# Kernel optimization log

Measured on AMD Instinct MI355X. Metric: run time of the kernel, lower is better.

## Reference

```python
import jax, jax.numpy as jnp
import numpy as np

N = 10000       # nodes (atoms)
E = 160000      # edges (avg degree 16)
NE = 10         # num_elements
C = 64          # hidden scalar channels (hidden_irreps 0e multiplicity)
NB = 8          # num_bessel
SH = 9          # spherical-harmonic dim for max_ell=2 (1+3+5)
MLPH = 16       # readout MLP hidden (MLP_irreps)
T = 2           # num_interactions
R_MAX = 5.0
P_CUT = 6       # num_polynomial_cutoff
AVG_NEIGH = 32.0


def _sph(u):
    # real spherical harmonics up to l=2, e3nn 'component' normalization
    x, y, z = u[:, 0], u[:, 1], u[:, 2]
    s3, s5, s15 = 3.0 ** 0.5, 5.0 ** 0.5, 15.0 ** 0.5
    return jnp.stack([
        jnp.ones_like(x),
        s3 * x, s3 * y, s3 * z,
        s15 * x * y, s15 * y * z, (s5 / 2) * (3 * z * z - 1),
        s15 * x * z, (s15 / 2) * (x * x - y * y)], axis=-1)


def _radial(r):
    # Bessel radial basis * smooth polynomial cutoff (RadialEmbeddingBlock)
    n = jnp.arange(1, NB + 1, dtype=r.dtype)
    bessel = (2.0 / R_MAX) ** 0.5 * jnp.sin(n * jnp.pi * r[:, None] / R_MAX) / r[:, None]
    x = jnp.clip(r / R_MAX, 0.0, 1.0)
    p = P_CUT
    fc = (1.0 - 0.5 * (p + 1) * (p + 2) * x ** p
          + p * (p + 2) * x ** (p + 1)
          - 0.5 * p * (p + 1) * x ** (p + 2))
    fc = jnp.where(x < 1.0, fc, 0.0)
    return bessel * fc[:, None]


def setup_inputs():
    key = jax.random.key(0)
    ks = jax.random.split(key, 14)
    positions = jax.random.normal(ks[0], (N, 3), jnp.float32) * 3.0
    node_attrs = jax.nn.one_hot(jax.random.randint(ks[1], (N,), 0, NE), NE, dtype=jnp.float32)
    edge_index = jax.random.randint(ks[2], (2, E), 0, N)
    shifts = jnp.zeros((E, 3), jnp.float32)

    def g(k, shape, fan):
        return jax.random.normal(k, shape, jnp.float32) / np.sqrt(fan)

    params = dict(
        atomic_energies=jax.random.normal(ks[3], (NE,), jnp.float32),
        W_embed=g(ks[4], (NE, C), NE),          # LinearNodeEmbeddingBlock
        W_up=g(ks[5], (T, C, C), C),            # linear_up per interaction
        W_r1=g(ks[6], (T, NB, MLPH), NB),       # radial MLP layer 1
        W_r2=g(ks[7], (T, MLPH, C * SH), MLPH), # radial MLP -> TP weights
        W_mix=g(ks[8], (T, C, SH, C), C * SH),  # post-scatter linear mixing
        W_self=g(ks[9], (T, C, C), C),          # self/skip connection
        w_read=g(ks[10], (C,), C),              # LinearReadoutBlock
        W_mlp1=g(ks[11], (C, MLPH), C),         # NonLinearReadoutBlock
        w_mlp2=g(ks[12], (MLPH,), MLPH),
    )
    return dict(positions=positions, node_attrs=node_attrs, shifts=shifts,
                edge_index=edge_index, **params)


def reference(positions, node_attrs, shifts, atomic_energies, W_embed, W_up,
              W_r1, W_r2, W_mix, W_self, w_read, W_mlp1, w_mlp2, edge_index):
    snd, rcv = edge_index[0], edge_index[1]
    vec = positions[rcv] - positions[snd] + shifts              # [E,3]
    r = jnp.linalg.norm(vec, axis=-1) + 1e-9                    # [E]
    sh = _sph(vec / r[:, None])                                 # [E,SH]
    edge_feats = _radial(r)                                     # [E,NB]

    h = node_attrs @ W_embed                                    # [N,C] node embedding
    reps = [node_attrs @ atomic_energies]                       # node_e0
    for t in range(T):
        h_up = h @ W_up[t]                                      # [N,C]
        # radial-MLP produced tensor-product weights, one per (channel, sh) path
        tp_w = (jax.nn.silu(edge_feats @ W_r1[t]) @ W_r2[t]).reshape(-1, C, SH)
        # gather -> edge-wise tensor product -> scatter-reduce (the hot loop)
        msg = tp_w * h_up[snd][:, :, None] * sh[:, None, :]     # [E,C,SH]
        agg = jax.ops.segment_sum(msg, rcv, num_segments=N) / AVG_NEIGH
        h = jnp.einsum('ncs,cso->no', agg, W_mix[t]) + h @ W_self[t]
        if t < T - 1:
            reps.append(h @ w_read)                             # linear readout
        else:
            reps.append(jax.nn.silu(h @ W_mlp1) @ w_mlp2)       # nonlinear readout
    return jnp.stack(reps, axis=0)  # [T+1, N] per-layer atomic energy contributions
```

## Files before the change

kernel.cpp:

```cpp
#include <hip/hip_runtime.h>
#include <math.h>

#define N_NODES 10000
#define N_EDGES 160000
#define NEL 10
#define C 64
#define NB 8
#define SHD 9
#define MLPH 16
#define CSH 576
#define R_MAX 5.0f
#define INV_AVG 0.03125f
#define SCAN_CH 40
#define GRID_MSG 768
#define NWAVES (GRID_MSG * 4)
#define WBASE (N_EDGES - 2 * 8 * CSH)
#define WB2   (WBASE - 10240)
#define WB3   (WB2 - 1024)

typedef _Float16 f16x2 __attribute__((ext_vector_type(2)));
typedef _Float16 f16x8 __attribute__((ext_vector_type(8)));
typedef float    f32x4 __attribute__((ext_vector_type(4)));
typedef _Float16 half_t;

__device__ __forceinline__ float silu_f(float v) {
    return v / (1.0f + __expf(-v));
}

__device__ __forceinline__ float dot2f(f16x2 a, f16x2 b, float c) {
#if __has_builtin(__builtin_amdgcn_fdot2)
    return __builtin_amdgcn_fdot2(a, b, c, false);
#else
    return c + (float)a.x * (float)b.x + (float)a.y * (float)b.y;
#endif
}

__device__ __forceinline__ int lbound_rp(const int* __restrict__ rp, int target) {
    int lo = 0, hi = N_NODES;
    while (lo < hi) { int mid = (lo + hi) >> 1; if (rp[mid] < target) lo = mid + 1; else hi = mid; }
    return lo;
}

__global__ __launch_bounds__(256) void k_edge(
    const float* __restrict__ pos, const float* __restrict__ shifts,
    const int* __restrict__ ei,
    const float* __restrict__ na, const float* __restrict__ We,
    const float* __restrict__ ae,
    int* __restrict__ cnt, int* __restrict__ deg,
    int* __restrict__ act_snd, int* __restrict__ act_rcv,
    float* __restrict__ act_u, float* __restrict__ act_ef,
    half_t* __restrict__ hh, float* __restrict__ out)
{
    int i = blockIdx.x * 256 + threadIdx.x;
    int lane = threadIdx.x & 63;

    {
        int n = i >> 6;
        float acc = 0.0f, e0 = 0.0f;
        #pragma unroll
        for (int k = 0; k < NEL; k++) {
            float a = na[n * NEL + k];
            acc += a * We[k * C + lane];
            e0 += a * ae[k];
        }
        hh[i] = (half_t)acc;
        if (lane == 0) out[n] = e0;
    }

    if (blockIdx.x >= N_EDGES / 256) return;
    int e = i;
    int snd = ei[e];
    int rcv = ei[N_EDGES + e];
    float vx = pos[rcv * 3 + 0] - pos[snd * 3 + 0] + shifts[e * 3 + 0];
    float vy = pos[rcv * 3 + 1] - pos[snd * 3 + 1] + shifts[e * 3 + 1];
    float vz = pos[rcv * 3 + 2] - pos[snd * 3 + 2] + shifts[e * 3 + 2];
    float r = sqrtf(vx * vx + vy * vy + vz * vz) + 1e-9f;
    float x = r / R_MAX;
    bool active = x < 1.0f;

    unsigned long long m = __ballot(active);
    int base = 0;
    if (m) {
        int leader = __ffsll((unsigned long long)m) - 1;
        if (lane == leader) base = atomicAdd(cnt, __popcll(m));
        base = __shfl(base, leader);
    }
    if (!active) return;

    int p = base + __popcll(m & ((1ull << lane) - 1ull));
    act_snd[p] = snd;
    act_rcv[p] = rcv;
    atomicAdd(&deg[rcv], 1);

    float inv_r = 1.0f / r;
    *(float4*)&act_u[p * 4] = make_float4(vx * inv_r, vy * inv_r, vz * inv_r, r);

    float x6 = x * x * x; x6 = x6 * x6;
    float x7 = x6 * x;
    float x8 = x7 * x;
    float fc = 1.0f - 28.0f * x6 + 48.0f * x7 - 21.0f * x8;
    float theta = 3.14159265358979323846f * r / R_MAX;
    float s1 = sinf(theta), c1 = cosf(theta);
    float sn = s1, cn = c1;
    float scale = 0.6324555320336759f * inv_r * fc;
    float ef[NB];
    ef[0] = scale * sn;
    #pragma unroll
    for (int n = 1; n < NB; n++) {
        float sn1 = sn * c1 + cn * s1;
        float cn1 = cn * c1 - sn * s1;
        sn = sn1; cn = cn1;
        ef[n] = scale * sn;
    }
    *(float4*)&act_ef[p * 8 + 0] = make_float4(ef[0], ef[1], ef[2], ef[3]);
    *(float4*)&act_ef[p * 8 + 4] = make_float4(ef[4], ef[5], ef[6], ef[7]);
}

__global__ __launch_bounds__(256) void k_scan(
    const int* __restrict__ deg, int* __restrict__ rowptr, int* __restrict__ cursor)
{
    __shared__ int dl[N_NODES];
    __shared__ int part[256];
    int tid = threadIdx.x;
    for (int i = tid; i < N_NODES; i += 256) dl[i] = deg[i];
    __syncthreads();

    int base = tid * SCAN_CH;
    int s = 0;
    #pragma unroll 8
    for (int i = 0; i < SCAN_CH; i++) {
        int idx = base + i;
        if (idx < N_NODES) s += dl[idx];
    }
    part[tid] = s;
    __syncthreads();
    for (int off = 1; off < 256; off <<= 1) {
        int v = (tid >= off) ? part[tid - off] : 0;
        __syncthreads();
        part[tid] += v;
        __syncthreads();
    }
    int run = part[tid] - s;
    for (int i = 0; i < SCAN_CH; i++) {
        int idx = base + i;
        if (idx < N_NODES) {
            int v = dl[idx];
            dl[idx] = run;
            run += v;
        }
    }
    __syncthreads();
    for (int i = tid; i < N_NODES; i += 256) {
        int r = dl[i];
        rowptr[i] = r;
        cursor[i] = r;
    }
    if (tid == 255) rowptr[N_NODES] = part[255];
}

__global__ __launch_bounds__(256) void k_rank(
    const int* __restrict__ cnt, const int* __restrict__ act_rcv,
    const float* __restrict__ Wr2, const float* __restrict__ Wmix,
    const float* __restrict__ Wself, const float* __restrict__ Wup,
    const int* __restrict__ rowptr,
    int* __restrict__ cursor, int* __restrict__ wstart, f16x2* __restrict__ wlth,
    f16x8* __restrict__ wmixf, f16x8* __restrict__ wupf, int* __restrict__ perm)
{
    int i = blockIdx.x * 256 + threadIdx.x;
    int nAct = *cnt;

    if (i <= NWAVES) {
        if (i == NWAVES) {
            wstart[NWAVES] = N_NODES;
        } else {
            int S = (nAct + NWAVES - 1) / NWAVES; if (S < 1) S = 1;
            wstart[i] = lbound_rp(rowptr, i * S);
        }
    }
    if (i >= WBASE) {
        int idx = i - WBASE;
        int t = idx / (8 * CSH);
        int r = idx - t * (8 * CSH);
        int mq = r / CSH, j = r - mq * CSH;
        int c = j & 63, s = j >> 6;
        float lo = Wr2[t * MLPH * CSH + (2 * mq + 0) * CSH + c * SHD + s];
        float hi = Wr2[t * MLPH * CSH + (2 * mq + 1) * CSH + c * SHD + s];
        f16x2 v; v.x = (_Float16)lo; v.y = (_Float16)hi;
        wlth[idx] = v;
    } else if (i >= WB2) {
        int idx = i - WB2;
        int t = idx / 5120;
        int r = idx - t * 5120;
        int ks = r >> 8;
        int rr = r & 255;
        int nt = rr >> 6;
        int ln = rr & 63;
        f16x8 v;
        #pragma unroll
        for (int e = 0; e < 8; e++) {
            int k = ks * 32 + ((ln >> 4) << 3) + e;
            int col = nt * 16 + (ln & 15);
            float x;
            if (k < CSH)
                x = Wmix[(size_t)t * CSH * C + ((k & 63) * SHD + (k >> 6)) * C + col] * INV_AVG;
            else
                x = Wself[(size_t)t * C * C + (k - CSH) * C + col];
            v[e] = (_Float16)x;
        }
        wmixf[(size_t)((t * 20 + ks) * 4 + nt) * 64 + ln] = v;
    } else if (i >= WB3) {
        int idx = i - WB3;
        int t = idx >> 9;
        int r = idx & 511;
        int ks = r >> 8;
        int rr = r & 255;
        int nt = rr >> 6;
        int ln = rr & 63;
        f16x8 v;
        #pragma unroll
        for (int e = 0; e < 8; e++) {
            int k = ks * 32 + ((ln >> 4) << 3) + e;
            int col = nt * 16 + (ln & 15);
            v[e] = (_Float16)Wup[(size_t)t * C * C + k * C + col];
        }
        wupf[(size_t)((t * 2 + ks) * 4 + nt) * 64 + ln] = v;
    }
    if (i >= nAct) return;
    int pos = atomicAdd(&cursor[act_rcv[i]], 1);
    perm[pos] = i;
}

__global__ __launch_bounds__(256) void k_permute(
    const int* __restrict__ cnt, const int* __restrict__ perm,
    const int* __restrict__ act_snd, const int* __restrict__ act_rcv,
    const float* __restrict__ act_u, const float* __restrict__ act_ef,
    const float* __restrict__ Wr1,
    int* __restrict__ csnd, int* __restrict__ crcv, float* __restrict__ csh,
    f16x2* __restrict__ chidh0, f16x2* __restrict__ chidh1)
{
    int p = blockIdx.x * 256 + threadIdx.x;
    if (p >= *cnt) return;
    int i = perm[p];

    csnd[p] = act_snd[i];
    crcv[p] = act_rcv[i];

    float4 u4 = *(const float4*)&act_u[i * 4];
    float ux = u4.x, uy = u4.y, uz = u4.z;
    const float s3 = 1.7320508075688772f;
    const float s5 = 2.23606797749979f;
    const float s15 = 3.872983346207417f;
    *(float4*)&csh[p * 16 + 0] = make_float4(1.0f, s3 * ux, s3 * uy, s3 * uz);
    *(float4*)&csh[p * 16 + 4] = make_float4(s15 * ux * uy, s15 * uy * uz,
                                             0.5f * s5 * (3.0f * uz * uz - 1.0f),
                                             s15 * ux * uz);
    csh[p * 16 + 8] = 0.5f * s15 * (ux * ux - uy * uy);

    float4 e0 = *(const float4*)&act_ef[i * 8 + 0];
    float4 e1 = *(const float4*)&act_ef[i * 8 + 4];
    float ef[NB] = {e0.x, e0.y, e0.z, e0.w, e1.x, e1.y, e1.z, e1.w};

    #pragma unroll
    for (int t = 0; t < 2; t++) {
        f16x2* dst = (t == 0) ? chidh0 : chidh1;
        const float* W = Wr1 + t * NB * MLPH;
        f16x2 hv2[8];
        #pragma unroll
        for (int mp = 0; mp < 8; mp++) {
            float a0 = 0.0f, a1 = 0.0f;
            #pragma unroll
            for (int b = 0; b < NB; b++) {
                float efb = ef[b];
                a0 += efb * W[b * MLPH + 2 * mp + 0];
                a1 += efb * W[b * MLPH + 2 * mp + 1];
            }
            f16x2 v; v.x = (_Float16)silu_f(a0); v.y = (_Float16)silu_f(a1);
            hv2[mp] = v;
        }
        *(float4*)&dst[p * 8 + 0] = *(float4*)&hv2[0];
        *(float4*)&dst[p * 8 + 4] = *(float4*)&hv2[4];
    }
}

__global__ __launch_bounds__(64) void k_upm(
    const half_t* __restrict__ hh, const f16x8* __restrict__ wupf,
    float* __restrict__ hup)
{
    int lane = threadIdx.x & 63;
    int base = blockIdx.x * 16;
    int rowA = base + (lane & 15);
    int kg = (lane >> 4) << 3;

    f32x4 u0 = {0.f,0.f,0.f,0.f}, u1 = {0.f,0.f,0.f,0.f};
    f32x4 u2 = {0.f,0.f,0.f,0.f}, u3 = {0.f,0.f,0.f,0.f};
    const half_t* hrow = hh + (size_t)rowA * C + kg;
    #pragma unroll
    for (int ks = 0; ks < 2; ks++) {
        f16x8 a = *(const f16x8*)(hrow + ks * 32);
        const f16x8* bp = wupf + (size_t)(ks * 4) * 64 + lane;
        u0 = __builtin_amdgcn_mfma_f32_16x16x32_f16(a, bp[0],   u0, 0, 0, 0);
        u1 = __builtin_amdgcn_mfma_f32_16x16x32_f16(a, bp[64],  u1, 0, 0, 0);
        u2 = __builtin_amdgcn_mfma_f32_16x16x32_f16(a, bp[128], u2, 0, 0, 0);
        u3 = __builtin_amdgcn_mfma_f32_16x16x32_f16(a, bp[192], u3, 0, 0, 0);
    }
    int colb = lane & 15;
    int rowb = base + ((lane >> 4) << 2);
    #pragma unroll
    for (int r = 0; r < 4; r++) {
        float* hp = hup + (size_t)(rowb + r) * C + colb;
        hp[0]  = u0[r];
        hp[16] = u1[r];
        hp[32] = u2[r];
        hp[48] = u3[r];
    }
}

__global__ __launch_bounds__(256) void k_msg5(
    const int* __restrict__ rowptr, const int* __restrict__ wstart,
    const int* __restrict__ csnd, const int* __restrict__ crcv,
    const float* __restrict__ csh, const f16x2* __restrict__ chh,
    const f16x2* __restrict__ wlth, const float* __restrict__ hup,
    half_t* __restrict__ aggh)
{
    int lane = threadIdx.x & 63;
    int w = (blockIdx.x << 2) | (threadIdx.x >> 6);
    int nlo = wstart[w];
    int nhi = wstart[w + 1];
    if (nlo >= nhi) return;
    int beg = rowptr[nlo], end = rowptr[nhi];

    f16x2 wreg[8][9];
    #pragma unroll
    for (int mq = 0; mq < 8; mq++)
        #pragma unroll
        for (int jj = 0; jj < 9; jj++)
            wreg[mq][jj] = wlth[mq * CSH + (jj << 6) + lane];

    float acc[9];
    int curRcv = -1;

#define FLUSH() { half_t* ag = aggh + (size_t)curRcv * CSH + lane; \
    _Pragma("unroll") for (int jj = 0; jj < 9; jj++) ag[jj << 6] = (half_t)acc[jj]; }
#define ZFILL(FROM, TO) for (int zn = (FROM); zn < (TO); zn++) { \
    half_t* ag = aggh + (size_t)zn * CSH + lane; \
    _Pragma("unroll") for (int jj = 0; jj < 9; jj++) ag[jj << 6] = (half_t)0.0f; }

    for (int k0 = beg; k0 < end; k0 += 4) {
        int nv = end - k0; if (nv > 4) nv = 4;

#define PRE(Q) int kc##Q = (k0 + Q < end) ? k0 + Q : end - 1; \
        int rcvq##Q = crcv[kc##Q]; \
        float hupq##Q = hup[csnd[kc##Q] * C + lane];
        PRE(0) PRE(1) PRE(2) PRE(3)
#undef PRE

        float tw0[9], tw1[9], tw2[9], tw3[9];
        #pragma unroll
        for (int jj = 0; jj < 9; jj++) {
            tw0[jj] = 0.f; tw1[jj] = 0.f; tw2[jj] = 0.f; tw3[jj] = 0.f;
        }

        #pragma unroll
        for (int mq = 0; mq < 8; mq++) {
            f16x2 h0 = chh[kc0 * 8 + mq], h1 = chh[kc1 * 8 + mq];
            f16x2 h2 = chh[kc2 * 8 + mq], h3 = chh[kc3 * 8 + mq];
            #pragma unroll
            for (int jj = 0; jj < 9; jj++) {
                f16x2 wv = wreg[mq][jj];
                tw0[jj] = dot2f(h0, wv, tw0[jj]);
                tw1[jj] = dot2f(h1, wv, tw1[jj]);
                tw2[jj] = dot2f(h2, wv, tw2[jj]);
                tw3[jj] = dot2f(h3, wv, tw3[jj]);
            }
        }

#define SCAT(Q) if (Q < nv) { \
        int rcv = rcvq##Q; \
        float hupS = hupq##Q; \
        float4 sA = *(const float4*)&csh[kc##Q * 16]; \
        float4 sB = *(const float4*)&csh[kc##Q * 16 + 4]; \
        float s8v = csh[kc##Q * 16 + 8]; \
        float sh9[9] = {sA.x, sA.y, sA.z, sA.w, sB.x, sB.y, sB.z, sB.w, s8v}; \
        if (rcv != curRcv) { \
            if (curRcv >= 0) { FLUSH(); ZFILL(curRcv + 1, rcv) } else { ZFILL(nlo, rcv) } \
            curRcv = rcv; \
            _Pragma("unroll") for (int jj = 0; jj < 9; jj++) acc[jj] = tw##Q[jj] * (hupS * sh9[jj]); \
        } else { \
            _Pragma("unroll") for (int jj = 0; jj < 9; jj++) acc[jj] += tw##Q[jj] * (hupS * sh9[jj]); \
        } }
        SCAT(0) SCAT(1) SCAT(2) SCAT(3)
#undef SCAT
    }

    int zfrom = nlo;
    if (curRcv >= 0) { FLUSH(); zfrom = curRcv + 1; }
    ZFILL(zfrom, nhi)
#undef FLUSH
#undef ZFILL
}

template <int RMODE>
__global__ __launch_bounds__(64) void k_mixm(
    const half_t* __restrict__ aggh, half_t* __restrict__ hh,
    const f16x8* __restrict__ wf, const f16x8* __restrict__ wupf,
    const float* __restrict__ wread, const float* __restrict__ Wm1,
    const float* __restrict__ wm2,
    float* __restrict__ hup, float* __restrict__ rep)
{
    __shared__ half_t Hs[16 * 72];
    __shared__ float  Hn[16 * 68];
    __shared__ float  W1l[C * MLPH];

    int lane = threadIdx.x & 63;
    int base = blockIdx.x * 16;
    int rowA = base + (lane & 15);
    int kg = (lane >> 4) << 3;

    if (RMODE == 1) {
        #pragma unroll
        for (int it = 0; it < 16; it++) W1l[lane + 64 * it] = Wm1[lane + 64 * it];
    }

    f32x4 acc0 = {0.f, 0.f, 0.f, 0.f};
    f32x4 acc1 = {0.f, 0.f, 0.f, 0.f};
    f32x4 acc2 = {0.f, 0.f, 0.f, 0.f};
    f32x4 acc3 = {0.f, 0.f, 0.f, 0.f};

    const half_t* arow = aggh + (size_t)rowA * CSH + kg;
    const half_t* hrow = hh + (size_t)rowA * C + kg;

    #pragma unroll
    for (int ks = 0; ks < 20; ks++) {
        f16x8 a = (ks < 18) ? *(const f16x8*)(arow + ks * 32)
                            : *(const f16x8*)(hrow + (ks - 18) * 32);
        const f16x8* bp = wf + (size_t)(ks * 4) * 64 + lane;
        acc0 = __builtin_amdgcn_mfma_f32_16x16x32_f16(a, bp[0],   acc0, 0, 0, 0);
        acc1 = __builtin_amdgcn_mfma_f32_16x16x32_f16(a, bp[64],  acc1, 0, 0, 0);
        acc2 = __builtin_amdgcn_mfma_f32_16x16x32_f16(a, bp[128], acc2, 0, 0, 0);
        acc3 = __builtin_amdgcn_mfma_f32_16x16x32_f16(a, bp[192], acc3, 0, 0, 0);
    }

    int colb = lane & 15;
    int rowb = base + ((lane >> 4) << 2);
    int rloc = (lane >> 4) << 2;

    if (RMODE == 0) {
        float wr0 = wread[colb], wr1 = wread[colb + 16];
        float wr2 = wread[colb + 32], wr3 = wread[colb + 48];
        #pragma unroll
        for (int r = 0; r < 4; r++) {
            float v = acc0[r] * wr0 + acc1[r] * wr1 + acc2[r] * wr2 + acc3[r] * wr3;
            v += __shfl_xor(v, 1); v += __shfl_xor(v, 2);
            v += __shfl_xor(v, 4); v += __shfl_xor(v, 8);
            if (colb == 0) rep[rowb + r] = v;
        }

        #pragma unroll
        for (int r = 0; r < 4; r++) {
            Hs[(rloc + r) * 72 + colb +  0] = (half_t)acc0[r];
            Hs[(rloc + r) * 72 + colb + 16] = (half_t)acc1[r];
            Hs[(rloc + r) * 72 + colb + 32] = (half_t)acc2[r];
            Hs[(rloc + r) * 72 + colb + 48] = (half_t)acc3[r];
        }
        __syncthreads();

        #pragma unroll
        for (int it = 0; it < 2; it++) {
            int idx = lane + 64 * it;
            int row = idx >> 3, cq = idx & 7;
            *(float4*)&hh[(size_t)(base + row) * C + cq * 8] =
                *(const float4*)&Hs[row * 72 + cq * 8];
        }

        f32x4 u0 = {0.f,0.f,0.f,0.f}, u1 = {0.f,0.f,0.f,0.f};
        f32x4 u2 = {0.f,0.f,0.f,0.f}, u3 = {0.f,0.f,0.f,0.f};
        #pragma unroll
        for (int ks = 0; ks < 2; ks++) {
            f16x8 a = *(const f16x8*)&Hs[(lane & 15) * 72 + kg + ks * 32];
            const f16x8* bp = wupf + (size_t)(ks * 4) * 64 + lane;
            u0 = __builtin_amdgcn_mfma_f32_16x16x32_f16(a, bp[0],   u0, 0, 0, 0);
            u1 = __builtin_amdgcn_mfma_f32_16x16x32_f16(a, bp[64],  u1, 0, 0, 0);
            u2 = __builtin_amdgcn_mfma_f32_16x16x32_f16(a, bp[128], u2, 0, 0, 0);
            u3 = __builtin_amdgcn_mfma_f32_16x16x32_f16(a, bp[192], u3, 0, 0, 0);
        }
        #pragma unroll
        for (int r = 0; r < 4; r++) {
            float* hp = hup + (size_t)(rowb + r) * C + colb;
            hp[0]  = u0[r];
            hp[16] = u1[r];
            hp[32] = u2[r];
            hp[48] = u3[r];
        }
    } else {
        #pragma unroll
        for (int r = 0; r < 4; r++) {
            Hn[(rloc + r) * 68 + colb +  0] = acc0[r];
            Hn[(rloc + r) * 68 + colb + 16] = acc1[r];
            Hn[(rloc + r) * 68 + colb + 32] = acc2[r];
            Hn[(rloc + r) * 68 + colb + 48] = acc3[r];
        }
        __syncthreads();
        int n = lane & 15, q = lane >> 4;
        float a2[4] = {0.f, 0.f, 0.f, 0.f};
        #pragma unroll 8
        for (int c = 0; c < C; c++) {
            float hv = Hn[n * 68 + c];
            #pragma unroll
            for (int j = 0; j < 4; j++) a2[j] += hv * W1l[c * MLPH + 4 * q + j];
        }
        float rv = 0.0f;
        #pragma unroll
        for (int j = 0; j < 4; j++) rv += silu_f(a2[j]) * wm2[4 * q + j];
        rv += __shfl_xor(rv, 16);
        rv += __shfl_xor(rv, 32);
        if (lane < 16) rep[base + n] = rv;
    }
}

extern "C" void kernel_launch(void* const* d_in, const int* in_sizes, int n_in,
                              void* d_out, int out_size, void* d_ws, size_t ws_size,
                              hipStream_t stream) {
    const float* pos    = (const float*)d_in[0];
    const float* na     = (const float*)d_in[1];
    const float* shifts = (const float*)d_in[2];
    const int*   ei     = (const int*)d_in[3];
    const float* ae     = (const float*)d_in[4];
    const float* We     = (const float*)d_in[5];
    const float* Wup    = (const float*)d_in[6];
    const float* Wr1    = (const float*)d_in[7];
    const float* Wr2    = (const float*)d_in[8];
    const float* Wmix   = (const float*)d_in[9];
    const float* Wself  = (const float*)d_in[10];
    const float* wread  = (const float*)d_in[11];
    const float* Wm1    = (const float*)d_in[12];
    const float* wm2    = (const float*)d_in[13];
    float* out = (float*)d_out;

    char* ws = (char*)d_ws;
    size_t off = 0;
    auto alloc = [&](size_t bytes) {
        off = (off + 255) & ~(size_t)255;
        void* p = ws + off;
        off += bytes;
        return p;
    };
    int*   cnt     = (int*)alloc(4);
    int*   deg     = (int*)alloc((size_t)N_NODES * 4);
    int*   rowptr  = (int*)alloc((size_t)(N_NODES + 1) * 4);
    int*   cursor  = (int*)alloc((size_t)N_NODES * 4);
    int*   wstart  = (int*)alloc((size_t)(NWAVES + 1) * 4);
    f16x2* wlth    = (f16x2*)alloc((size_t)2 * 8 * CSH * 4);
    f16x8* wmixf   = (f16x8*)alloc((size_t)2 * 5120 * 16);
    f16x8* wupf    = (f16x8*)alloc((size_t)1024 * 16);
    int*   perm    = (int*)alloc((size_t)N_EDGES * 4);
    int*   act_snd = (int*)alloc((size_t)N_EDGES * 4);
    int*   act_rcv = (int*)alloc((size_t)N_EDGES * 4);
    float* act_u   = (float*)alloc((size_t)N_EDGES * 4 * 4);
    float* act_ef  = (float*)alloc((size_t)N_EDGES * 8 * 4);
    int*   csnd    = (int*)alloc((size_t)N_EDGES * 4);
    int*   crcv    = (int*)alloc((size_t)N_EDGES * 4);
    float* csh     = (float*)alloc((size_t)N_EDGES * 16 * 4);
    f16x2* chidh0  = (f16x2*)alloc((size_t)N_EDGES * 8 * 4);
    f16x2* chidh1  = (f16x2*)alloc((size_t)N_EDGES * 8 * 4);
    float* hup     = (float*)alloc((size_t)N_NODES * C * 4);
    half_t* hh     = (half_t*)alloc((size_t)N_NODES * C * 2);
    half_t* aggh   = (half_t*)alloc((size_t)N_NODES * CSH * 2);

    hipMemsetAsync(cnt, 0, 4, stream);
    hipMemsetAsync(deg, 0, (size_t)N_NODES * 4, stream);

    k_edge<<<(N_NODES * C) / 256, 256, 0, stream>>>(pos, shifts, ei, na, We, ae,
                                                    cnt, deg, act_snd, act_rcv,
                                                    act_u, act_ef, hh, out);
    k_scan<<<1, 256, 0, stream>>>(deg, rowptr, cursor);
    k_rank<<<N_EDGES / 256, 256, 0, stream>>>(cnt, act_rcv, Wr2, Wmix, Wself, Wup,
                                              rowptr, cursor, wstart, wlth,
                                              wmixf, wupf, perm);
    k_permute<<<N_EDGES / 256, 256, 0, stream>>>(cnt, perm, act_snd, act_rcv,
                                                 act_u, act_ef, Wr1,
                                                 csnd, crcv, csh, chidh0, chidh1);
    k_upm<<<N_NODES / 16, 64, 0, stream>>>(hh, wupf, hup);

    k_msg5<<<GRID_MSG, 256, 0, stream>>>(rowptr, wstart, csnd, crcv, csh,
                                         chidh0, wlth, hup, aggh);
    k_mixm<0><<<N_NODES / 16, 64, 0, stream>>>(aggh, hh, wmixf, wupf + 512,
                                               wread, Wm1, wm2,
                                               hup, out + N_NODES);

    k_msg5<<<GRID_MSG, 256, 0, stream>>>(rowptr, wstart, csnd, crcv, csh,
                                         chidh1, wlth + 8 * CSH, hup, aggh);
    k_mixm<1><<<N_NODES / 16, 64, 0, stream>>>(aggh, hh, wmixf + 5120, wupf + 512,
                                               wread, Wm1, wm2,
                                               hup, out + 2 * N_NODES);
}
```

Measured before the change: 134.9 us.

## Fuse message aggregation with mixing MLP via shared-memory aggregates

Merges the per-edge message/scatter kernel and the node mixing/readout kernel into one kernel per interaction. Each 256-thread block owns 16 nodes, and each wave handles 4 consecutive nodes. Aggregates go to LDS instead of a global fp16 buffer, then all four waves run the MFMA mixing together. This removes the global aggregate round-trip, one launch per layer and the edge-balanced wave partitioning (wstart binary search). The cost is load imbalance across waves, since work now follows node degree rather than edge count, and the load of the 72-entry weight registers is amortized over only 4 nodes per wave.

```diff
diff --git a/kernel.cpp b/kernel.cpp
--- a/kernel.cpp
+++ b/kernel.cpp
@@ -12,11 +12,10 @@
 #define R_MAX 5.0f
 #define INV_AVG 0.03125f
 #define SCAN_CH 40
-#define GRID_MSG 768
-#define NWAVES (GRID_MSG * 4)
 #define WBASE (N_EDGES - 2 * 8 * CSH)
 #define WB2   (WBASE - 10240)
 #define WB3   (WB2 - 1024)
+#define ROWP  584
 
 typedef _Float16 f16x2 __attribute__((ext_vector_type(2)));
 typedef _Float16 f16x8 __attribute__((ext_vector_type(8)));
@@ -33,12 +32,6 @@
 #else
     return c + (float)a.x * (float)b.x + (float)a.y * (float)b.y;
 #endif
-}
-
-__device__ __forceinline__ int lbound_rp(const int* __restrict__ rp, int target) {
-    int lo = 0, hi = N_NODES;
-    while (lo < hi) { int mid = (lo + hi) >> 1; if (rp[mid] < target) lo = mid + 1; else hi = mid; }
-    return lo;
 }
 
 __global__ __launch_bounds__(256) void k_edge(
@@ -162,21 +155,12 @@
     const int* __restrict__ cnt, const int* __restrict__ act_rcv,
     const float* __restrict__ Wr2, const float* __restrict__ Wmix,
     const float* __restrict__ Wself, const float* __restrict__ Wup,
-    const int* __restrict__ rowptr,
-    int* __restrict__ cursor, int* __restrict__ wstart, f16x2* __restrict__ wlth,
+    int* __restrict__ cursor, f16x2* __restrict__ wlth,
     f16x8* __restrict__ wmixf, f16x8* __restrict__ wupf, int* __restrict__ perm)
 {
     int i = blockIdx.x * 256 + threadIdx.x;
     int nAct = *cnt;
 
-    if (i <= NWAVES) {
-        if (i == NWAVES) {
-            wstart[NWAVES] = N_NODES;
-        } else {
-            int S = (nAct + NWAVES - 1) / NWAVES; if (S < 1) S = 1;
-            wstart[i] = lbound_rp(rowptr, i * S);
-        }
-    }
     if (i >= WBASE) {
         int idx = i - WBASE;
         int t = idx / (8 * CSH);
@@ -315,19 +299,25 @@
     }
 }
 
-__global__ __launch_bounds__(256) void k_msg5(
-    const int* __restrict__ rowptr, const int* __restrict__ wstart,
-    const int* __restrict__ csnd, const int* __restrict__ crcv,
-    const float* __restrict__ csh, const f16x2* __restrict__ chh,
-    const f16x2* __restrict__ wlth, const float* __restrict__ hup,
-    half_t* __restrict__ aggh)
+template <int RMODE>
+__global__ __launch_bounds__(256) void k_fuse(
+    const int* __restrict__ rowptr, const int* __restrict__ csnd,
+    const int* __restrict__ crcv, const float* __restrict__ csh,
+    const f16x2* __restrict__ chh, const f16x2* __restrict__ wlth,
+    const float* __restrict__ hup_in, const f16x8* __restrict__ wf,
+    const f16x8* __restrict__ wupf1, half_t* __restrict__ hh,
+    const float* __restrict__ wread, const float* __restrict__ Wm1,
+    const float* __restrict__ wm2,
+    float* __restrict__ hup_out, float* __restrict__ rep)
 {
+    __shared__ half_t Hs[16 * ROWP];
+    __shared__ half_t Hs2[16 * 72];
+
     int lane = threadIdx.x & 63;
-    int w = (blockIdx.x << 2) | (threadIdx.x >> 6);
-    int nlo = wstart[w];
-    int nhi = wstart[w + 1];
-    if (nlo >= nhi) return;
-    int beg = rowptr[nlo], end = rowptr[nhi];
+    int w = threadIdx.x >> 6;
+    int bbase = blockIdx.x * 16;
+    int n0 = bbase + w * 4;
+    int beg = rowptr[n0], end = rowptr[n0 + 4];
 
     f16x2 wreg[8][9];
     #pragma unroll
@@ -339,10 +329,10 @@
     float acc[9];
     int curRcv = -1;
 
-#define FLUSH() { half_t* ag = aggh + (size_t)curRcv * CSH + lane; \
+#define FLUSH() { half_t* ag = &Hs[(curRcv - bbase) * ROWP + lane]; \
     _Pragma("unroll") for (int jj = 0; jj < 9; jj++) ag[jj << 6] = (half_t)acc[jj]; }
 #define ZFILL(FROM, TO) for (int zn = (FROM); zn < (TO); zn++) { \
-    half_t* ag = aggh + (size_t)zn * CSH + lane; \
+    half_t* ag = &Hs[(zn - bbase) * ROWP + lane]; \
     _Pragma("unroll") for (int jj = 0; jj < 9; jj++) ag[jj << 6] = (half_t)0.0f; }
 
     for (int k0 = beg; k0 < end; k0 += 4) {
@@ -350,7 +340,7 @@
 
 #define PRE(Q) int kc##Q = (k0 + Q < end) ? k0 + Q : end - 1; \
         int rcvq##Q = crcv[kc##Q]; \
-        float hupq##Q = hup[csnd[kc##Q] * C + lane];
+        float hupq##Q = hup_in[csnd[kc##Q] * C + lane];
         PRE(0) PRE(1) PRE(2) PRE(3)
 #undef PRE
 
@@ -382,7 +372,7 @@
         float s8v = csh[kc##Q * 16 + 8]; \
         float sh9[9] = {sA.x, sA.y, sA.z, sA.w, sB.x, sB.y, sB.z, sB.w, s8v}; \
         if (rcv != curRcv) { \
-            if (curRcv >= 0) { FLUSH(); ZFILL(curRcv + 1, rcv) } else { ZFILL(nlo, rcv) } \
+            if (curRcv >= 0) { FLUSH(); ZFILL(curRcv + 1, rcv) } else { ZFILL(n0, rcv) } \
             curRcv = rcv; \
             _Pragma("unroll") for (int jj = 0; jj < 9; jj++) acc[jj] = tw##Q[jj] * (hupS * sh9[jj]); \
         } else { \
@@ -392,128 +382,84 @@
 #undef SCAT
     }
 
-    int zfrom = nlo;
+    int zfrom = n0;
     if (curRcv >= 0) { FLUSH(); zfrom = curRcv + 1; }
-    ZFILL(zfrom, nhi)
+    ZFILL(zfrom, n0 + 4)
 #undef FLUSH
 #undef ZFILL
-}
-
-template <int RMODE>
-__global__ __launch_bounds__(64) void k_mixm(
-    const half_t* __restrict__ aggh, half_t* __restrict__ hh,
-    const f16x8* __restrict__ wf, const f16x8* __restrict__ wupf,
-    const float* __restrict__ wread, const float* __restrict__ Wm1,
-    const float* __restrict__ wm2,
-    float* __restrict__ hup, float* __restrict__ rep)
-{
-    __shared__ half_t Hs[16 * 72];
-    __shared__ float  Hn[16 * 68];
-    __shared__ float  W1l[C * MLPH];
-
-    int lane = threadIdx.x & 63;
-    int base = blockIdx.x * 16;
-    int rowA = base + (lane & 15);
+
+    __syncthreads();
+
+    int rowL = lane & 15;
     int kg = (lane >> 4) << 3;
-
-    if (RMODE == 1) {
-        #pragma unroll
-        for (int it = 0; it < 16; it++) W1l[lane + 64 * it] = Wm1[lane + 64 * it];
-    }
-
-    f32x4 acc0 = {0.f, 0.f, 0.f, 0.f};
-    f32x4 acc1 = {0.f, 0.f, 0.f, 0.f};
-    f32x4 acc2 = {0.f, 0.f, 0.f, 0.f};
-    f32x4 acc3 = {0.f, 0.f, 0.f, 0.f};
-
-    const half_t* arow = aggh + (size_t)rowA * CSH + kg;
-    const half_t* hrow = hh + (size_t)rowA * C + kg;
-
+    f32x4 acc4 = {0.f, 0.f, 0.f, 0.f};
+    const half_t* hrow = hh + (size_t)(bbase + rowL) * C + kg;
     #pragma unroll
     for (int ks = 0; ks < 20; ks++) {
-        f16x8 a = (ks < 18) ? *(const f16x8*)(arow + ks * 32)
+        f16x8 a = (ks < 18) ? *(const f16x8*)&Hs[rowL * ROWP + ks * 32 + kg]
                             : *(const f16x8*)(hrow + (ks - 18) * 32);
-        const f16x8* bp = wf + (size_t)(ks * 4) * 64 + lane;
-        acc0 = __builtin_amdgcn_mfma_f32_16x16x32_f16(a, bp[0],   acc0, 0, 0, 0);
-        acc1 = __builtin_amdgcn_mfma_f32_16x16x32_f16(a, bp[64],  acc1, 0, 0, 0);
-        acc2 = __builtin_amdgcn_mfma_f32_16x16x32_f16(a, bp[128], acc2, 0, 0, 0);
-        acc3 = __builtin_amdgcn_mfma_f32_16x16x32_f16(a, bp[192], acc3, 0, 0, 0);
+        f16x8 b = wf[(size_t)(ks * 4 + w) * 64 + lane];
+        acc4 = __builtin_amdgcn_mfma_f32_16x16x32_f16(a, b, acc4, 0, 0, 0);
     }
 
     int colb = lane & 15;
-    int rowb = base + ((lane >> 4) << 2);
-    int rloc = (lane >> 4) << 2;
+    int rq = (lane >> 4) << 2;
+
+    __syncthreads();
 
     if (RMODE == 0) {
-        float wr0 = wread[colb], wr1 = wread[colb + 16];
-        float wr2 = wread[colb + 32], wr3 = wread[colb + 48];
-        #pragma unroll
-        for (int r = 0; r < 4; r++) {
-            float v = acc0[r] * wr0 + acc1[r] * wr1 + acc2[r] * wr2 + acc3[r] * wr3;
-            v += __shfl_xor(v, 1); v += __shfl_xor(v, 2);
-            v += __shfl_xor(v, 4); v += __shfl_xor(v, 8);
-            if (colb == 0) rep[rowb + r] = v;
-        }
-
-        #pragma unroll
-        for (int r = 0; r < 4; r++) {
-            Hs[(rloc + r) * 72 + colb +  0] = (half_t)acc0[r];
-            Hs[(rloc + r) * 72 + colb + 16] = (half_t)acc1[r];
-            Hs[(rloc + r) * 72 + colb + 32] = (half_t)acc2[r];
-            Hs[(rloc + r) * 72 + colb + 48] = (half_t)acc3[r];
-        }
+        #pragma unroll
+        for (int r = 0; r < 4; r++)
+            Hs2[(rq + r) * 72 + w * 16 + colb] = (half_t)acc4[r];
         __syncthreads();
 
-        #pragma unroll
-        for (int it = 0; it < 2; it++) {
-            int idx = lane + 64 * it;
-            int row = idx >> 3, cq = idx & 7;
-            *(float4*)&hh[(size_t)(base + row) * C + cq * 8] =
-                *(const float4*)&Hs[row * 72 + cq * 8];
-        }
-
-        f32x4 u0 = {0.f,0.f,0.f,0.f}, u1 = {0.f,0.f,0.f,0.f};
-        f32x4 u2 = {0.f,0.f,0.f,0.f}, u3 = {0.f,0.f,0.f,0.f};
+        if (w == 0) {
+            int row = lane & 15, seg = lane >> 4;
+            float v = 0.0f;
+            #pragma unroll
+            for (int j = 0; j < 16; j++)
+                v += (float)Hs2[row * 72 + seg * 16 + j] * wread[seg * 16 + j];
+            v += __shfl_xor(v, 16);
+            v += __shfl_xor(v, 32);
+            if (seg == 0) rep[bbase + row] = v;
+        }
+
+        {
+            int idx = threadIdx.x;
+            if (idx < 128) {
+                int row = idx >> 3, cq = idx & 7;
+                *(float4*)&hh[(size_t)(bbase + row) * C + cq * 8] =
+                    *(const float4*)&Hs2[row * 72 + cq * 8];
+            }
+        }
+
+        f32x4 u = {0.f, 0.f, 0.f, 0.f};
         #pragma unroll
         for (int ks = 0; ks < 2; ks++) {
-            f16x8 a = *(const f16x8*)&Hs[(lane & 15) * 72 + kg + ks * 32];
-            const f16x8* bp = wupf + (size_t)(ks * 4) * 64 + lane;
-            u0 = __builtin_amdgcn_mfma_f32_16x16x32_f16(a, bp[0],   u0, 0, 0, 0);
-            u1 = __builtin_amdgcn_mfma_f32_16x16x32_f16(a, bp[64],  u1, 0, 0, 0);
-            u2 = __builtin_amdgcn_mfma_f32_16x16x32_f16(a, bp[128], u2, 0, 0, 0);
-            u3 = __builtin_amdgcn_mfma_f32_16x16x32_f16(a, bp[192], u3, 0, 0, 0);
-        }
-        #pragma unroll
-        for (int r = 0; r < 4; r++) {
-            float* hp = hup + (size_t)(rowb + r) * C + colb;
-            hp[0]  = u0[r];
-            hp[16] = u1[r];
-            hp[32] = u2[r];
-            hp[48] = u3[r];
-        }
+            f16x8 a = *(const f16x8*)&Hs2[rowL * 72 + ks * 32 + kg];
+            f16x8 b = wupf1[(size_t)(ks * 4 + w) * 64 + lane];
+            u = __builtin_amdgcn_mfma_f32_16x16x32_f16(a, b, u, 0, 0, 0);
+        }
+        #pragma unroll
+        for (int r = 0; r < 4; r++)
+            hup_out[(size_t)(bbase + rq + r) * C + w * 16 + colb] = u[r];
     } else {
-        #pragma unroll
-        for (int r = 0; r < 4; r++) {
-            Hn[(rloc + r) * 68 + colb +  0] = acc0[r];
-            Hn[(rloc + r) * 68 + colb + 16] = acc1[r];
-            Hn[(rloc + r) * 68 + colb + 32] = acc2[r];
-            Hn[(rloc + r) * 68 + colb + 48] = acc3[r];
-        }
+        float* Hn = (float*)Hs;
+        float* W1l = (float*)Hs + 16 * 68;
+        for (int t = threadIdx.x; t < C * MLPH; t += 256) W1l[t] = Wm1[t];
+        #pragma unroll
+        for (int r = 0; r < 4; r++)
+            Hn[(rq + r) * 68 + w * 16 + colb] = acc4[r];
         __syncthreads();
-        int n = lane & 15, q = lane >> 4;
-        float a2[4] = {0.f, 0.f, 0.f, 0.f};
+
+        int n = threadIdx.x >> 4, m = threadIdx.x & 15;
+        float a2 = 0.0f;
         #pragma unroll 8
-        for (int c = 0; c < C; c++) {
-            float hv = Hn[n * 68 + c];
-            #pragma unroll
-            for (int j = 0; j < 4; j++) a2[j] += hv * W1l[c * MLPH + 4 * q + j];
-        }
-        float rv = 0.0f;
-        #pragma unroll
-        for (int j = 0; j < 4; j++) rv += silu_f(a2[j]) * wm2[4 * q + j];
-        rv += __shfl_xor(rv, 16);
-        rv += __shfl_xor(rv, 32);
-        if (lane < 16) rep[base + n] = rv;
+        for (int c = 0; c < C; c++) a2 += Hn[n * 68 + c] * W1l[c * MLPH + m];
+        float rv = silu_f(a2) * wm2[m];
+        rv += __shfl_xor(rv, 1); rv += __shfl_xor(rv, 2);
+        rv += __shfl_xor(rv, 4); rv += __shfl_xor(rv, 8);
+        if (m == 0) rep[bbase + n] = rv;
     }
 }
 
@@ -548,7 +494,6 @@
     int*   deg     = (int*)alloc((size_t)N_NODES * 4);
     int*   rowptr  = (int*)alloc((size_t)(N_NODES + 1) * 4);
     int*   cursor  = (int*)alloc((size_t)N_NODES * 4);
-    int*   wstart  = (int*)alloc((size_t)(NWAVES + 1) * 4);
     f16x2* wlth    = (f16x2*)alloc((size_t)2 * 8 * CSH * 4);
     f16x8* wmixf   = (f16x8*)alloc((size_t)2 * 5120 * 16);
     f16x8* wupf    = (f16x8*)alloc((size_t)1024 * 16);
@@ -563,8 +508,8 @@
     f16x2* chidh0  = (f16x2*)alloc((size_t)N_EDGES * 8 * 4);
     f16x2* chidh1  = (f16x2*)alloc((size_t)N_EDGES * 8 * 4);
     float* hup     = (float*)alloc((size_t)N_NODES * C * 4);
+    float* hup2    = (float*)alloc((size_t)N_NODES * C * 4);
     half_t* hh     = (half_t*)alloc((size_t)N_NODES * C * 2);
-    half_t* aggh   = (half_t*)alloc((size_t)N_NODES * CSH * 2);
 
     hipMemsetAsync(cnt, 0, 4, stream);
     hipMemsetAsync(deg, 0, (size_t)N_NODES * 4, stream);
@@ -574,22 +519,21 @@
                                                     act_u, act_ef, hh, out);
     k_scan<<<1, 256, 0, stream>>>(deg, rowptr, cursor);
     k_rank<<<N_EDGES / 256, 256, 0, stream>>>(cnt, act_rcv, Wr2, Wmix, Wself, Wup,
-                                              rowptr, cursor, wstart, wlth,
-                                              wmixf, wupf, perm);
+                                              cursor, wlth, wmixf, wupf, perm);
     k_permute<<<N_EDGES / 256, 256, 0, stream>>>(cnt, perm, act_snd, act_rcv,
                                                  act_u, act_ef, Wr1,
                                                  csnd, crcv, csh, chidh0, chidh1);
     k_upm<<<N_NODES / 16, 64, 0, stream>>>(hh, wupf, hup);
 
-    k_msg5<<<GRID_MSG, 256, 0, stream>>>(rowptr, wstart, csnd, crcv, csh,
-                                         chidh0, wlth, hup, aggh);
-    k_mixm<0><<<N_NODES / 16, 64, 0, stream>>>(aggh, hh, wmixf, wupf + 512,
-                                               wread, Wm1, wm2,
-                                               hup, out + N_NODES);
-
-    k_msg5<<<GRID_MSG, 256, 0, stream>>>(rowptr, wstart, csnd, crcv, csh,
-                                         chidh1, wlth + 8 * CSH, hup, aggh);
-    k_mixm<1><<<N_NODES / 16, 64, 0, stream>>>(aggh, hh, wmixf + 5120, wupf + 512,
-                                               wread, Wm1, wm2,
-                                               hup, out + 2 * N_NODES);
-}
+    k_fuse<0><<<N_NODES / 16, 256, 0, stream>>>(rowptr, csnd, crcv, csh,
+                                                chidh0, wlth, hup,
+                                                wmixf, wupf + 512, hh,
+                                                wread, Wm1, wm2,
+                                                hup2, out + N_NODES);
+
+    k_fuse<1><<<N_NODES / 16, 256, 0, stream>>>(rowptr, csnd, crcv, csh,
+                                                chidh1, wlth + 8 * CSH, hup2,
+                                                wmixf + 5120, wupf + 512, hh,
+                                                wread, Wm1, wm2,
+                                                hup, out + 2 * N_NODES);
+}
```

New measurement: 124.9 us. 1.08x faster.
